# Optimization experiments

Hardware: AMD Instinct MI355X
Metric: run time of the kernel (lower is better)

The kernel has to match this reference:

```python
import jax, jax.numpy as jnp
import numpy as np

B, NA, NT, P, DA, DM, H = 1, 4096, 1024, 32768, 128, 512, 4
DH = DA // H
DF = 4 * DA
WINDOW = 16


def _layer_norm(x, g=None, b=None, eps=1e-5):
    m = jnp.mean(x, axis=-1, keepdims=True)
    v = jnp.var(x, axis=-1, keepdims=True)
    xn = (x - m) / jnp.sqrt(v + eps)
    if g is not None:
        xn = xn * g + b
    return xn


def setup_inputs() -> dict:
    key = jax.random.key(0)
    ks = jax.random.split(key, 32)
    r = lambda k, s: (jax.random.normal(k, s, dtype=jnp.float32) * 0.05)
    return {
        'q': r(ks[0], (B, NA, DA)),
        'c_atom': r(ks[1], (B, NA, DA)),
        'h_cond': r(ks[2], (B, NT, DM)),
        'p_lm': r(ks[3], (B, P, 16)),
        't_emb': r(ks[4], (B, DA)),
        'cond_proj_w': r(ks[5], (DM, DA)), 'cond_proj_b': r(ks[6], (DA,)),
        'adaln1_w': r(ks[7], (DA, 2 * DA)), 'adaln1_b': r(ks[8], (2 * DA,)),
        'adaln2_w': r(ks[9], (DA, 2 * DA)), 'adaln2_b': r(ks[10], (2 * DA,)),
        'ln_g': jnp.ones((DA,), jnp.float32), 'ln_b': jnp.zeros((DA,), jnp.float32),
        'wq': r(ks[11], (DA, DA)), 'wk': r(ks[12], (DA, DA)),
        'wv': r(ks[13], (DA, DA)), 'wg': r(ks[14], (DA, DA)),
        'wo': r(ks[15], (DA, DA)),
        'pair_w': r(ks[16], (16, H)), 'pair_b': r(ks[17], (H,)),
        'gate1_w': r(ks[18], (DA, DA)), 'gate1_b': r(ks[19], (DA,)),
        'gate2_w': r(ks[20], (DA, DA)), 'gate2_b': r(ks[21], (DA,)),
        'sw1': r(ks[22], (DA, DF)), 'sw3': r(ks[23], (DA, DF)),
        'sw2': r(ks[24], (DF, DA)),
        'p_lm_idx': jax.random.randint(ks[25], (B, P, 2), 0, NA, dtype=jnp.int32),
        'token_idx': jnp.sort(jax.random.randint(ks[26], (B, NA), 0, NT, dtype=jnp.int32), axis=-1),
    }


def _forward(q, c_atom, h_cond, p_lm, t_emb,
             cond_proj_w, cond_proj_b, adaln1_w, adaln1_b, adaln2_w, adaln2_b,
             ln_g, ln_b, wq, wk, wv, wg, wo, pair_w, pair_b,
             gate1_w, gate1_b, gate2_w, gate2_b, sw1, sw3, sw2,
             p_lm_idx, token_idx):
    Bq, N, D = q.shape
    # gather token conditioning to atoms: (B, NA, DM)
    h_atoms = jax.vmap(lambda h, t: h[t])(h_cond, token_idx)
    cond = t_emb[:, None, :] + h_atoms @ cond_proj_w + cond_proj_b  # (B, NA, DA)
    g1, b1 = jnp.split(cond @ adaln1_w + adaln1_b, 2, axis=-1)
    q_n = (1.0 + g1) * _layer_norm(q, ln_g, ln_b) + b1

    Q = (q_n @ wq).reshape(Bq, N, H, DH)
    K = (q_n @ wk).reshape(Bq, N, H, DH)
    V = (q_n @ wv).reshape(Bq, N, H, DH)
    G_flat = q_n @ wg  # (B, N, DA); permute/reshape in torch is identity on layout

    scores = jnp.einsum('bihd,bjhd->bhij', Q, K) / jnp.sqrt(jnp.float32(DH))

    # scattered pair bias: (B, P, H) -> dense (B, H, N, N)
    bias = p_lm @ pair_w + pair_b  # (B, P, H)

    def scat(idx, bb):
        return jnp.zeros((N, N, H), bb.dtype).at[idx[:, 0], idx[:, 1]].set(bb)

    pair_bias = jax.vmap(scat)(p_lm_idx, bias).transpose(0, 3, 1, 2)
    scores = scores + pair_bias

    pos = jnp.arange(N)
    window = jnp.abs(pos[:, None] - pos[None, :]) <= WINDOW  # (N, N)
    scores = jnp.where(window[None, None, :, :], scores, -jnp.inf)

    attn = jax.nn.softmax(scores, axis=-1)
    att_out = jnp.einsum('bhij,bjhd->bihd', attn, V).reshape(Bq, N, D)

    q1 = q + jax.nn.sigmoid(G_flat) * (att_out @ wo)
    q1 = q1 + jax.nn.sigmoid(c_atom @ gate1_w + gate1_b) * q1

    g2, b2 = jnp.split(cond @ adaln2_w + adaln2_b, 2, axis=-1)
    q_n2 = (1.0 + g2) * _layer_norm(q1) + b2
    swi = (jax.nn.silu(q_n2 @ sw1) * (q_n2 @ sw3)) @ sw2
    q2 = q1 + jax.nn.sigmoid(c_atom @ gate2_w + gate2_b) * swi
    return q2  # atom_pad_mask is all-ones -> final mask multiply is identity


def reference(q, c_atom, h_cond, p_lm, t_emb,
              cond_proj_w, cond_proj_b, adaln1_w, adaln1_b, adaln2_w, adaln2_b,
              ln_g, ln_b, wq, wk, wv, wg, wo, pair_w, pair_b,
              gate1_w, gate1_b, gate2_w, gate2_b, sw1, sw3, sw2,
              p_lm_idx, token_idx):
    return _forward(q, c_atom, h_cond, p_lm, t_emb,
                    cond_proj_w, cond_proj_b, adaln1_w, adaln1_b, adaln2_w, adaln2_b,
                    ln_g, ln_b, wq, wk, wv, wg, wo, pair_w, pair_b,
                    gate1_w, gate1_b, gate2_w, gate2_b, sw1, sw3, sw2,
                    p_lm_idx, token_idx)
```

## Files before the change

kernel.cpp:

```cpp
#include <hip/hip_runtime.h>
#include <math.h>

#define NA   4096
#define DA   128
#define DM   512
#define NT   1024
#define HH   4
#define DF   512
#define PP   32768
#define WIN  16
#define BAND 33
#define KSTR 132

typedef __attribute__((ext_vector_type(8))) short bf16x8;
typedef __attribute__((ext_vector_type(4))) float f32x4;

__device__ __forceinline__ float sigmoidf_(float x) { return 1.0f / (1.0f + __expf(-x)); }
__device__ __forceinline__ ushort f2bf(float f) {
    union { float f; unsigned int i; } x; x.f = f;
    unsigned int r = x.i + 0x7fffu + ((x.i >> 16) & 1u);
    return (ushort)(r >> 16);
}

__global__ __launch_bounds__(256) void k_prep(
    const float* __restrict__ hc, const float* __restrict__ ca,
    const float* __restrict__ cw, const float* __restrict__ a1, const float* __restrict__ a2,
    const float* __restrict__ wq, const float* __restrict__ wk, const float* __restrict__ wv,
    const float* __restrict__ wg, const float* __restrict__ wo,
    const float* __restrict__ g1, const float* __restrict__ g2,
    const float* __restrict__ s1, const float* __restrict__ s3, const float* __restrict__ s2,
    ushort* hcb, ushort* cab, ushort* cwT, ushort* a1T, ushort* a2T,
    ushort* wqT, ushort* wkT, ushort* wvT, ushort* wgT, ushort* woT,
    ushort* g1T, ushort* g2T, ushort* s1T, ushort* s3T, ushort* s2T,
    float* band)
{
    __shared__ float tile[32][33];
    const int y = blockIdx.y, bx = blockIdx.x, tid = threadIdx.x;
    if (y <= 1) {
        const float4* src = (const float4*)(y == 0 ? hc : ca);
        ushort* dst = y == 0 ? hcb : cab;
        for (int i = bx * 256 + tid; i < 131072; i += 16384) {
            float4 v = src[i];
            ushort4 st; st.x = f2bf(v.x); st.y = f2bf(v.y); st.z = f2bf(v.z); st.w = f2bf(v.w);
            *(ushort4*)&dst[(size_t)i * 4] = st;
        }
        return;
    }
    if (y == 15) {
        float4 z = {0.f, 0.f, 0.f, 0.f};
        float4* b4 = (float4*)band;
        for (int i = bx * 256 + tid; i < 135168; i += 16384) b4[i] = z;
        return;
    }
    const float* src; ushort* dst; int K, N;
    switch (y) {
        case 2:  src = cw; dst = cwT; K = 512; N = 128; break;
        case 3:  src = a1; dst = a1T; K = 128; N = 256; break;
        case 4:  src = a2; dst = a2T; K = 128; N = 256; break;
        case 5:  src = wq; dst = wqT; K = 128; N = 128; break;
        case 6:  src = wk; dst = wkT; K = 128; N = 128; break;
        case 7:  src = wv; dst = wvT; K = 128; N = 128; break;
        case 8:  src = wg; dst = wgT; K = 128; N = 128; break;
        case 9:  src = wo; dst = woT; K = 128; N = 128; break;
        case 10: src = g1; dst = g1T; K = 128; N = 128; break;
        case 11: src = g2; dst = g2T; K = 128; N = 128; break;
        case 12: src = s1; dst = s1T; K = 128; N = 512; break;
        case 13: src = s3; dst = s3T; K = 128; N = 512; break;
        default: src = s2; dst = s2T; K = 512; N = 128; break;
    }
    const int tn_cnt = N >> 5;
    if (bx >= (K >> 5) * tn_cnt) return;
    const int k0 = (bx / tn_cnt) << 5, n0 = (bx % tn_cnt) << 5;
    {
        int r = tid >> 3, c = (tid & 7) << 2;
        float4 v = *(const float4*)&src[(size_t)(k0 + r) * N + n0 + c];
        tile[r][c + 0] = v.x; tile[r][c + 1] = v.y;
        tile[r][c + 2] = v.z; tile[r][c + 3] = v.w;
    }
    __syncthreads();
    {
        int rn = tid >> 3, ck = (tid & 7) << 2;
        ushort4 st;
        st.x = f2bf(tile[ck + 0][rn]);
        st.y = f2bf(tile[ck + 1][rn]);
        st.z = f2bf(tile[ck + 2][rn]);
        st.w = f2bf(tile[ck + 3][rn]);
        *(ushort4*)&dst[(size_t)(n0 + rn) * K + k0 + ck] = st;
    }
}

__global__ __launch_bounds__(256) void k_condmod(
    const ushort* __restrict__ hcb, const int* __restrict__ tok,
    const ushort* __restrict__ cwT, const float* __restrict__ t_emb,
    const float* __restrict__ cond_b, const ushort* __restrict__ cab,
    const ushort* __restrict__ a1T, const ushort* __restrict__ a2T,
    const ushort* __restrict__ g1T, const ushort* __restrict__ g2T,
    const float* __restrict__ ad1b, const float* __restrict__ ad2b,
    const float* __restrict__ g1b, const float* __restrict__ g2b,
    const float* __restrict__ p_lm, const float* __restrict__ pair_w,
    const float* __restrict__ pair_b, const int* __restrict__ p_idx,
    float* __restrict__ band,
    float* __restrict__ gb1, float* __restrict__ gb2,
    float* __restrict__ gate1, float* __restrict__ gate2)
{
    const int tid = threadIdx.x, b = blockIdx.x;
    if (b >= 256) {
        int p = (b - 256) * 256 + tid;
        int i = p_idx[2 * p], j = p_idx[2 * p + 1];
        int d = j - i + WIN;
        if (d < 0 || d > 2 * WIN) return;
        float v0 = pair_b[0], v1 = pair_b[1], v2 = pair_b[2], v3 = pair_b[3];
        #pragma unroll
        for (int k = 0; k < 16; ++k) {
            float a = p_lm[p * 16 + k];
            v0 = fmaf(a, pair_w[k * 4 + 0], v0);
            v1 = fmaf(a, pair_w[k * 4 + 1], v1);
            v2 = fmaf(a, pair_w[k * 4 + 2], v2);
            v3 = fmaf(a, pair_w[k * 4 + 3], v3);
        }
        size_t base = ((size_t)i * HH) * BAND + d;
        band[base + 0 * BAND] = v0;
        band[base + 1 * BAND] = v1;
        band[base + 2 * BAND] = v2;
        band[base + 3 * BAND] = v3;
        return;
    }
    __shared__ ushort cond_s[16 * 128];
    const int l = tid & 63, wv = tid >> 6;
    const int cl = l & 15, kq = l >> 4, ko = kq * 8;
    const int r0 = b * 16;
    {
        const int n0 = wv * 32;
        const ushort* Arow = hcb + (size_t)tok[r0 + cl] * DM;
        const ushort* Wc = cwT + (size_t)(n0 + cl) * DM;
        f32x4 acc[2] = {};
        #pragma unroll
        for (int ks = 0; ks < 16; ++ks) {
            bf16x8 a = *(const bf16x8*)(Arow + ks * 32 + ko);
            #pragma unroll
            for (int nf = 0; nf < 2; ++nf) {
                bf16x8 bb = *(const bf16x8*)(Wc + (size_t)nf * 16 * DM + ks * 32 + ko);
                acc[nf] = __builtin_amdgcn_mfma_f32_16x16x32_bf16(a, bb, acc[nf], 0, 0, 0);
            }
        }
        #pragma unroll
        for (int nf = 0; nf < 2; ++nf) {
            int col = n0 + nf * 16 + cl;
            float add = t_emb[col] + cond_b[col];
            #pragma unroll
            for (int r = 0; r < 4; ++r) {
                int row = kq * 4 + r;
                int byte = row * 256 + col * 2;
                byte ^= (row & 7) << 4;
                *(ushort*)((char*)cond_s + byte) = f2bf(acc[nf][r] + add);
            }
        }
    }
    __syncthreads();
    {
        const int n0 = wv * 64;
        const ushort* W1c = a1T + (size_t)(n0 + cl) * DA;
        const ushort* W2c = a2T + (size_t)(n0 + cl) * DA;
        f32x4 acc1[4] = {}, acc2[4] = {};
        #pragma unroll
        for (int ks = 0; ks < 4; ++ks) {
            int byteA = cl * 256 + (ks * 32 + ko) * 2;
            byteA ^= (cl & 7) << 4;
            bf16x8 a = *(const bf16x8*)((char*)cond_s + byteA);
            #pragma unroll
            for (int nf = 0; nf < 4; ++nf) {
                bf16x8 b1 = *(const bf16x8*)(W1c + (size_t)nf * 16 * DA + ks * 32 + ko);
                acc1[nf] = __builtin_amdgcn_mfma_f32_16x16x32_bf16(a, b1, acc1[nf], 0, 0, 0);
                bf16x8 b2 = *(const bf16x8*)(W2c + (size_t)nf * 16 * DA + ks * 32 + ko);
                acc2[nf] = __builtin_amdgcn_mfma_f32_16x16x32_bf16(a, b2, acc2[nf], 0, 0, 0);
            }
        }
        #pragma unroll
        for (int nf = 0; nf < 4; ++nf) {
            int col = n0 + nf * 16 + cl;
            float b1v = ad1b[col], b2v = ad2b[col];
            #pragma unroll
            for (int r = 0; r < 4; ++r) {
                size_t rc = (size_t)(r0 + kq * 4 + r) * 256 + col;
                gb1[rc] = acc1[nf][r] + b1v;
                gb2[rc] = acc2[nf][r] + b2v;
            }
        }
    }
    {
        const int n0 = wv * 32;
        const ushort* Arow = cab + (size_t)(r0 + cl) * DA;
        const ushort* W1c = g1T + (size_t)(n0 + cl) * DA;
        const ushort* W2c = g2T + (size_t)(n0 + cl) * DA;
        f32x4 acc1[2] = {}, acc2[2] = {};
        #pragma unroll
        for (int ks = 0; ks < 4; ++ks) {
            bf16x8 a = *(const bf16x8*)(Arow + ks * 32 + ko);
            #pragma unroll
            for (int nf = 0; nf < 2; ++nf) {
                bf16x8 b1 = *(const bf16x8*)(W1c + (size_t)nf * 16 * DA + ks * 32 + ko);
                acc1[nf] = __builtin_amdgcn_mfma_f32_16x16x32_bf16(a, b1, acc1[nf], 0, 0, 0);
                bf16x8 b2 = *(const bf16x8*)(W2c + (size_t)nf * 16 * DA + ks * 32 + ko);
                acc2[nf] = __builtin_amdgcn_mfma_f32_16x16x32_bf16(a, b2, acc2[nf], 0, 0, 0);
            }
        }
        #pragma unroll
        for (int nf = 0; nf < 2; ++nf) {
            int col = n0 + nf * 16 + cl;
            float b1v = g1b[col], b2v = g2b[col];
            #pragma unroll
            for (int r = 0; r < 4; ++r) {
                size_t rc = (size_t)(r0 + kq * 4 + r) * DA + col;
                gate1[rc] = sigmoidf_(acc1[nf][r] + b1v);
                gate2[rc] = sigmoidf_(acc2[nf][r] + b2v);
            }
        }
    }
}

__global__ __launch_bounds__(512) void k_mega(
    const float* __restrict__ qg, const float* __restrict__ gb1,
    const float* __restrict__ gb2, const float* __restrict__ gate1,
    const float* __restrict__ gate2, const float* __restrict__ ln_g,
    const float* __restrict__ ln_b, const float* __restrict__ band,
    const ushort* __restrict__ wqT, const ushort* __restrict__ wkT,
    const ushort* __restrict__ wvT, const ushort* __restrict__ wgT,
    const ushort* __restrict__ woT, const ushort* __restrict__ s1T,
    const ushort* __restrict__ s3T, const ushort* __restrict__ s2T,
    float* __restrict__ out)
{
    __shared__ ushort qn_s[48 * 128];
    __shared__ float  K_s[48 * KSTR];
    __shared__ float  V_s[48 * KSTR];
    __shared__ float  Q_s[16 * KSTR];
    __shared__ float  sG_s[16 * KSTR];
    __shared__ float  q1_s[16 * KSTR];
    __shared__ ushort att_s[16 * 128];
    __shared__ ushort hb_s[16 * 512];

    const int tid = threadIdx.x;
    const int l = tid & 63, wv = tid >> 6;
    const int cl = l & 15, kq = l >> 4, ko = kq * 8;
    const int r0 = blockIdx.x * 16;
    const int hb0 = r0 - 16;

    #pragma unroll
    for (int rr = 0; rr < 6; ++rr) {
        int hr = wv * 6 + rr;
        int gr = hb0 + hr;
        ushort2 st = {0, 0};
        if ((unsigned)gr < NA) {
            float2 xv = *(const float2*)&qg[(size_t)gr * DA + 2 * l];
            float sum = xv.x + xv.y, sq = xv.x * xv.x + xv.y * xv.y;
            #pragma unroll
            for (int off = 1; off <= 32; off <<= 1) {
                sum += __shfl_xor(sum, off);
                sq  += __shfl_xor(sq,  off);
            }
            float m = sum * (1.0f / DA);
            float rs = rsqrtf(sq * (1.0f / DA) - m * m + 1e-5f);
            float2 g = *(const float2*)&gb1[(size_t)gr * 256 + 2 * l];
            float2 bb = *(const float2*)&gb1[(size_t)gr * 256 + 128 + 2 * l];
            float2 lg = *(const float2*)&ln_g[2 * l];
            float2 lb = *(const float2*)&ln_b[2 * l];
            float xn0 = (xv.x - m) * rs * lg.x + lb.x;
            float xn1 = (xv.y - m) * rs * lg.y + lb.y;
            st.x = f2bf((1.f + g.x) * xn0 + bb.x);
            st.y = f2bf((1.f + g.y) * xn1 + bb.y);
        }
        int byte = hr * 256 + 4 * l;
        byte ^= (hr & 7) << 4;
        *(ushort2*)((char*)qn_s + byte) = st;
    }
    __syncthreads();

    {
        int t, isV = 0;
        const ushort* WT;
        if (wv < 6) { t = wv >> 1; isV = wv & 1; WT = isV ? wvT : wkT; }
        else        { t = 1; WT = (wv == 6) ? wqT : wgT; }
        const ushort* Wc = WT + (size_t)cl * DA;
        f32x4 acc[8] = {};
        #pragma unroll
        for (int ks = 0; ks < 4; ++ks) {
            int byteA = (t * 16 + cl) * 256 + (ks * 32 + ko) * 2;
            byteA ^= (cl & 7) << 4;
            bf16x8 a = *(const bf16x8*)((char*)qn_s + byteA);
            #pragma unroll
            for (int nf = 0; nf < 8; ++nf) {
                bf16x8 b = *(const bf16x8*)(Wc + (size_t)nf * 16 * DA + ks * 32 + ko);
                acc[nf] = __builtin_amdgcn_mfma_f32_16x16x32_bf16(a, b, acc[nf], 0, 0, 0);
            }
        }
        if (wv < 6) {
            float* dst = isV ? V_s : K_s;
            #pragma unroll
            for (int nf = 0; nf < 8; ++nf)
                #pragma unroll
                for (int r = 0; r < 4; ++r)
                    dst[(t * 16 + kq * 4 + r) * KSTR + nf * 16 + cl] = acc[nf][r];
        } else if (wv == 6) {
            #pragma unroll
            for (int nf = 0; nf < 8; ++nf)
                #pragma unroll
                for (int r = 0; r < 4; ++r)
                    Q_s[(kq * 4 + r) * KSTR + nf * 16 + cl] = acc[nf][r];
        } else {
            #pragma unroll
            for (int nf = 0; nf < 8; ++nf)
                #pragma unroll
                for (int r = 0; r < 4; ++r)
                    sG_s[(kq * 4 + r) * KSTR + nf * 16 + cl] = sigmoidf_(acc[nf][r]);
        }
    }
    __syncthreads();

    {
        const int g = tid >> 3, l3 = tid & 7;
        const int rl = g >> 2, h = g & 3;
        const int gr = r0 + rl;
        const float scale = 0.17677669529663687f;
        float4 qr0 = *(const float4*)&Q_s[rl * KSTR + h * 32 + l3 * 4];
        const float* brow = band + ((size_t)gr * HH + h) * BAND;
        float s[BAND];
        float m = -1e30f;
        #pragma unroll
        for (int jo = 0; jo < BAND; ++jo) {
            int j = gr - WIN + jo;
            float sv = -1e30f;
            if ((unsigned)j < NA) {
                float4 kk = *(const float4*)&K_s[(rl + jo) * KSTR + h * 32 + l3 * 4];
                float d = 0.f;
                d = fmaf(qr0.x, kk.x, d); d = fmaf(qr0.y, kk.y, d);
                d = fmaf(qr0.z, kk.z, d); d = fmaf(qr0.w, kk.w, d);
                d += __shfl_xor(d, 1);
                d += __shfl_xor(d, 2);
                d += __shfl_xor(d, 4);
                sv = fmaf(d, scale, brow[jo]);
            }
            s[jo] = sv;
            m = fmaxf(m, sv);
        }
        float lsum = 0.f;
        #pragma unroll
        for (int jo = 0; jo < BAND; ++jo) {
            float p = __expf(s[jo] - m);
            s[jo] = p;
            lsum += p;
        }
        float inv = 1.0f / lsum;
        float4 o = {0.f, 0.f, 0.f, 0.f};
        #pragma unroll
        for (int jo = 0; jo < BAND; ++jo) {
            int j = gr - WIN + jo;
            if ((unsigned)j < NA) {
                float4 v = *(const float4*)&V_s[(rl + jo) * KSTR + h * 32 + l3 * 4];
                o.x = fmaf(s[jo], v.x, o.x);
                o.y = fmaf(s[jo], v.y, o.y);
                o.z = fmaf(s[jo], v.z, o.z);
                o.w = fmaf(s[jo], v.w, o.w);
            }
        }
        ushort4 st;
        st.x = f2bf(o.x * inv); st.y = f2bf(o.y * inv);
        st.z = f2bf(o.z * inv); st.w = f2bf(o.w * inv);
        int byte = rl * 256 + h * 64 + l3 * 8;
        byte ^= (rl & 7) << 4;
        *(ushort4*)((char*)att_s + byte) = st;
    }
    __syncthreads();

    {
        const int n0 = wv * 16;
        const ushort* Wc = woT + (size_t)(n0 + cl) * DA;
        f32x4 acc = {0.f, 0.f, 0.f, 0.f};
        #pragma unroll
        for (int ks = 0; ks < 4; ++ks) {
            int byteA = cl * 256 + (ks * 32 + ko) * 2;
            byteA ^= (cl & 7) << 4;
            bf16x8 a = *(const bf16x8*)((char*)att_s + byteA);
            bf16x8 b = *(const bf16x8*)(Wc + ks * 32 + ko);
            acc = __builtin_amdgcn_mfma_f32_16x16x32_bf16(a, b, acc, 0, 0, 0);
        }
        #pragma unroll
        for (int r = 0; r < 4; ++r) {
            int row = kq * 4 + r;
            int gr = r0 + row, col = n0 + cl;
            float qv = qg[(size_t)gr * DA + col];
            float sg = sG_s[row * KSTR + col];
            float g1v = gate1[(size_t)gr * DA + col];
            q1_s[row * KSTR + col] = (qv + sg * acc[r]) * (1.f + g1v);
        }
    }
    __syncthreads();

    bf16x8 afr[4];
    {
        const int row = cl, gr = r0 + cl;
        float qv2[4][8];
        float sum = 0.f, sq = 0.f;
        #pragma unroll
        for (int ks = 0; ks < 4; ++ks) {
            float4 v0 = *(const float4*)&q1_s[row * KSTR + ks * 32 + ko];
            float4 v1 = *(const float4*)&q1_s[row * KSTR + ks * 32 + ko + 4];
            qv2[ks][0] = v0.x; qv2[ks][1] = v0.y; qv2[ks][2] = v0.z; qv2[ks][3] = v0.w;
            qv2[ks][4] = v1.x; qv2[ks][5] = v1.y; qv2[ks][6] = v1.z; qv2[ks][7] = v1.w;
            sum += v0.x + v0.y + v0.z + v0.w + v1.x + v1.y + v1.z + v1.w;
            sq += v0.x * v0.x + v0.y * v0.y + v0.z * v0.z + v0.w * v0.w
                + v1.x * v1.x + v1.y * v1.y + v1.z * v1.z + v1.w * v1.w;
        }
        sum += __shfl_xor(sum, 16); sq += __shfl_xor(sq, 16);
        sum += __shfl_xor(sum, 32); sq += __shfl_xor(sq, 32);
        float mean = sum * (1.0f / DA);
        float rs = rsqrtf(sq * (1.0f / DA) - mean * mean + 1e-5f);
        #pragma unroll
        for (int ks = 0; ks < 4; ++ks) {
            int k = ks * 32 + ko;
            float4 g0 = *(const float4*)&gb2[(size_t)gr * 256 + k];
            float4 g1v = *(const float4*)&gb2[(size_t)gr * 256 + k + 4];
            float4 b0 = *(const float4*)&gb2[(size_t)gr * 256 + 128 + k];
            float4 b1v = *(const float4*)&gb2[(size_t)gr * 256 + 128 + k + 4];
            float gg[8] = {g0.x, g0.y, g0.z, g0.w, g1v.x, g1v.y, g1v.z, g1v.w};
            float bb[8] = {b0.x, b0.y, b0.z, b0.w, b1v.x, b1v.y, b1v.z, b1v.w};
            #pragma unroll
            for (int j = 0; j < 8; ++j) {
                float xn = (qv2[ks][j] - mean) * rs;
                afr[ks][j] = (short)f2bf((1.f + gg[j]) * xn + bb[j]);
            }
        }
    }

    {
        const int c0 = wv * 64;
        const ushort* W1 = s1T + (size_t)(c0 + cl) * DA;
        const ushort* W3 = s3T + (size_t)(c0 + cl) * DA;
        f32x4 acc1[4] = {}, acc3[4] = {};
        #pragma unroll
        for (int ks = 0; ks < 4; ++ks) {
            #pragma unroll
            for (int nf = 0; nf < 4; ++nf) {
                bf16x8 b1 = *(const bf16x8*)(W1 + (size_t)nf * 16 * DA + ks * 32 + ko);
                acc1[nf] = __builtin_amdgcn_mfma_f32_16x16x32_bf16(afr[ks], b1, acc1[nf], 0, 0, 0);
                bf16x8 b3 = *(const bf16x8*)(W3 + (size_t)nf * 16 * DA + ks * 32 + ko);
                acc3[nf] = __builtin_amdgcn_mfma_f32_16x16x32_bf16(afr[ks], b3, acc3[nf], 0, 0, 0);
            }
        }
        #pragma unroll
        for (int nf = 0; nf < 4; ++nf) {
            #pragma unroll
            for (int r = 0; r < 4; ++r) {
                float x1 = acc1[nf][r], x3 = acc3[nf][r];
                float h = x1 * sigmoidf_(x1) * x3;
                int rr = kq * 4 + r;
                int col = c0 + nf * 16 + cl;
                int byte = rr * 1024 + col * 2;
                byte ^= (rr & 7) << 4;
                *(ushort*)((char*)hb_s + byte) = f2bf(h);
            }
        }
    }
    __syncthreads();
    {
        const int n0 = wv * 16;
        const ushort* W2 = s2T + (size_t)(n0 + cl) * DF;
        f32x4 acc = {0.f, 0.f, 0.f, 0.f};
        #pragma unroll
        for (int ks = 0; ks < 16; ++ks) {
            int byteA = cl * 1024 + (ks * 32 + ko) * 2;
            byteA ^= (cl & 7) << 4;
            bf16x8 a = *(const bf16x8*)((char*)hb_s + byteA);
            bf16x8 b = *(const bf16x8*)(W2 + ks * 32 + ko);
            acc = __builtin_amdgcn_mfma_f32_16x16x32_bf16(a, b, acc, 0, 0, 0);
        }
        #pragma unroll
        for (int r = 0; r < 4; ++r) {
            int row = kq * 4 + r;
            int gr = r0 + row, col = n0 + cl;
            size_t rc = (size_t)gr * DA + col;
            out[rc] = q1_s[row * KSTR + col] + gate2[rc] * acc[r];
        }
    }
}

extern "C" void kernel_launch(void* const* d_in, const int* in_sizes, int n_in,
                              void* d_out, int out_size, void* d_ws, size_t ws_size,
                              hipStream_t stream)
{
    const float* q      = (const float*)d_in[0];
    const float* c_atom = (const float*)d_in[1];
    const float* h_cond = (const float*)d_in[2];
    const float* p_lm   = (const float*)d_in[3];
    const float* t_emb  = (const float*)d_in[4];
    const float* cond_w = (const float*)d_in[5];
    const float* cond_b = (const float*)d_in[6];
    const float* ad1w   = (const float*)d_in[7];
    const float* ad1b   = (const float*)d_in[8];
    const float* ad2w   = (const float*)d_in[9];
    const float* ad2b   = (const float*)d_in[10];
    const float* ln_g   = (const float*)d_in[11];
    const float* ln_b   = (const float*)d_in[12];
    const float* wq     = (const float*)d_in[13];
    const float* wk     = (const float*)d_in[14];
    const float* wv     = (const float*)d_in[15];
    const float* wg     = (const float*)d_in[16];
    const float* wo     = (const float*)d_in[17];
    const float* pair_w = (const float*)d_in[18];
    const float* pair_b = (const float*)d_in[19];
    const float* g1w    = (const float*)d_in[20];
    const float* g1b    = (const float*)d_in[21];
    const float* g2w    = (const float*)d_in[22];
    const float* g2b    = (const float*)d_in[23];
    const float* sw1    = (const float*)d_in[24];
    const float* sw3    = (const float*)d_in[25];
    const float* sw2    = (const float*)d_in[26];
    const int*   p_idx  = (const int*)d_in[27];
    const int*   tok    = (const int*)d_in[28];
    float* out = (float*)d_out;

    size_t off = 0;
    char* base = (char*)d_ws;
    auto alloc = [&](size_t bytes) -> void* {
        void* p = base + off;
        off += (bytes + 255) & ~(size_t)255;
        return p;
    };
    ushort* hcb     = (ushort*)alloc((size_t)NT * DM * 2);
    ushort* cab     = (ushort*)alloc((size_t)NA * DA * 2);
    ushort* cwT     = (ushort*)alloc((size_t)DM * DA * 2);
    ushort* a1T     = (ushort*)alloc((size_t)256 * 128 * 2);
    ushort* a2T     = (ushort*)alloc((size_t)256 * 128 * 2);
    ushort* wqT     = (ushort*)alloc((size_t)128 * 128 * 2);
    ushort* wkT     = (ushort*)alloc((size_t)128 * 128 * 2);
    ushort* wvT     = (ushort*)alloc((size_t)128 * 128 * 2);
    ushort* wgT     = (ushort*)alloc((size_t)128 * 128 * 2);
    ushort* woT     = (ushort*)alloc((size_t)128 * 128 * 2);
    ushort* g1T     = (ushort*)alloc((size_t)128 * 128 * 2);
    ushort* g2T     = (ushort*)alloc((size_t)128 * 128 * 2);
    ushort* s1T     = (ushort*)alloc((size_t)512 * 128 * 2);
    ushort* s3T     = (ushort*)alloc((size_t)512 * 128 * 2);
    ushort* s2T     = (ushort*)alloc((size_t)128 * 512 * 2);
    float*  gb1     = (float*)alloc((size_t)NA * 256 * 4);
    float*  gb2     = (float*)alloc((size_t)NA * 256 * 4);
    float*  gate1   = (float*)alloc((size_t)NA * DA * 4);
    float*  gate2   = (float*)alloc((size_t)NA * DA * 4);
    float*  band    = (float*)alloc((size_t)NA * HH * BAND * 4);

    k_prep<<<dim3(64, 16), 256, 0, stream>>>(
        h_cond, c_atom, cond_w, ad1w, ad2w, wq, wk, wv, wg, wo,
        g1w, g2w, sw1, sw3, sw2,
        hcb, cab, cwT, a1T, a2T, wqT, wkT, wvT, wgT, woT,
        g1T, g2T, s1T, s3T, s2T, band);
    k_condmod<<<384, 256, 0, stream>>>(
        hcb, tok, cwT, t_emb, cond_b, cab,
        a1T, a2T, g1T, g2T, ad1b, ad2b, g1b, g2b,
        p_lm, pair_w, pair_b, p_idx, band,
        gb1, gb2, gate1, gate2);
    k_mega<<<256, 512, 0, stream>>>(
        q, gb1, gb2, gate1, gate2, ln_g, ln_b, band,
        wqT, wkT, wvT, wgT, woT, s1T, s3T, s2T, out);
    (void)in_sizes; (void)n_in; (void)out_size; (void)ws_size;
}
```

Measured before the change: 168.5 us.

## Fuse input bf16 conversion into condmod, store adaLN in bf16, stage mega inputs in LDS

Drops the separate h_cond/c_atom bf16 conversion pass in k_prep and converts fp32 rows on the fly inside k_condmod. The adaLN gamma/beta intermediates are written as bf16 to halve their traffic. k_mega now bulk-loads q, gb1/gb2, gates and band rows into a large shared pool up front, stores K/V as bf16 in LDS, and splits LayerNorm into a stats pass plus a vectorized normalize pass. The ~160KB LDS pool limits occupancy to one block per CU and adds precision loss in the adaLN and K/V values.

```diff
diff --git a/kernel.cpp b/kernel.cpp
--- a/kernel.cpp
+++ b/kernel.cpp
@@ -10,7 +10,6 @@
 #define PP   32768
 #define WIN  16
 #define BAND 33
-#define KSTR 132
 
 typedef __attribute__((ext_vector_type(8))) short bf16x8;
 typedef __attribute__((ext_vector_type(4))) float f32x4;
@@ -21,32 +20,27 @@
     unsigned int r = x.i + 0x7fffu + ((x.i >> 16) & 1u);
     return (ushort)(r >> 16);
 }
+__device__ __forceinline__ float bf2f(ushort u) {
+    union { unsigned int i; float f; } x; x.i = ((unsigned int)u) << 16;
+    return x.f;
+}
+
+#define MFMA(a, b, c) __builtin_amdgcn_mfma_f32_16x16x32_bf16((a), (b), (c), 0, 0, 0)
 
 __global__ __launch_bounds__(256) void k_prep(
-    const float* __restrict__ hc, const float* __restrict__ ca,
     const float* __restrict__ cw, const float* __restrict__ a1, const float* __restrict__ a2,
     const float* __restrict__ wq, const float* __restrict__ wk, const float* __restrict__ wv,
     const float* __restrict__ wg, const float* __restrict__ wo,
     const float* __restrict__ g1, const float* __restrict__ g2,
     const float* __restrict__ s1, const float* __restrict__ s3, const float* __restrict__ s2,
-    ushort* hcb, ushort* cab, ushort* cwT, ushort* a1T, ushort* a2T,
+    ushort* cwT, ushort* a1T, ushort* a2T,
     ushort* wqT, ushort* wkT, ushort* wvT, ushort* wgT, ushort* woT,
     ushort* g1T, ushort* g2T, ushort* s1T, ushort* s3T, ushort* s2T,
     float* band)
 {
     __shared__ float tile[32][33];
     const int y = blockIdx.y, bx = blockIdx.x, tid = threadIdx.x;
-    if (y <= 1) {
-        const float4* src = (const float4*)(y == 0 ? hc : ca);
-        ushort* dst = y == 0 ? hcb : cab;
-        for (int i = bx * 256 + tid; i < 131072; i += 16384) {
-            float4 v = src[i];
-            ushort4 st; st.x = f2bf(v.x); st.y = f2bf(v.y); st.z = f2bf(v.z); st.w = f2bf(v.w);
-            *(ushort4*)&dst[(size_t)i * 4] = st;
-        }
-        return;
-    }
-    if (y == 15) {
+    if (y == 13) {
         float4 z = {0.f, 0.f, 0.f, 0.f};
         float4* b4 = (float4*)band;
         for (int i = bx * 256 + tid; i < 135168; i += 16384) b4[i] = z;
@@ -54,18 +48,18 @@
     }
     const float* src; ushort* dst; int K, N;
     switch (y) {
-        case 2:  src = cw; dst = cwT; K = 512; N = 128; break;
-        case 3:  src = a1; dst = a1T; K = 128; N = 256; break;
-        case 4:  src = a2; dst = a2T; K = 128; N = 256; break;
-        case 5:  src = wq; dst = wqT; K = 128; N = 128; break;
-        case 6:  src = wk; dst = wkT; K = 128; N = 128; break;
-        case 7:  src = wv; dst = wvT; K = 128; N = 128; break;
-        case 8:  src = wg; dst = wgT; K = 128; N = 128; break;
-        case 9:  src = wo; dst = woT; K = 128; N = 128; break;
-        case 10: src = g1; dst = g1T; K = 128; N = 128; break;
-        case 11: src = g2; dst = g2T; K = 128; N = 128; break;
-        case 12: src = s1; dst = s1T; K = 128; N = 512; break;
-        case 13: src = s3; dst = s3T; K = 128; N = 512; break;
+        case 0:  src = cw; dst = cwT; K = 512; N = 128; break;
+        case 1:  src = a1; dst = a1T; K = 128; N = 256; break;
+        case 2:  src = a2; dst = a2T; K = 128; N = 256; break;
+        case 3:  src = wq; dst = wqT; K = 128; N = 128; break;
+        case 4:  src = wk; dst = wkT; K = 128; N = 128; break;
+        case 5:  src = wv; dst = wvT; K = 128; N = 128; break;
+        case 6:  src = wg; dst = wgT; K = 128; N = 128; break;
+        case 7:  src = wo; dst = woT; K = 128; N = 128; break;
+        case 8:  src = g1; dst = g1T; K = 128; N = 128; break;
+        case 9:  src = g2; dst = g2T; K = 128; N = 128; break;
+        case 10: src = s1; dst = s1T; K = 128; N = 512; break;
+        case 11: src = s3; dst = s3T; K = 128; N = 512; break;
         default: src = s2; dst = s2T; K = 512; N = 128; break;
     }
     const int tn_cnt = N >> 5;
@@ -90,9 +84,9 @@
 }
 
 __global__ __launch_bounds__(256) void k_condmod(
-    const ushort* __restrict__ hcb, const int* __restrict__ tok,
+    const float* __restrict__ h_cond, const int* __restrict__ tok,
     const ushort* __restrict__ cwT, const float* __restrict__ t_emb,
-    const float* __restrict__ cond_b, const ushort* __restrict__ cab,
+    const float* __restrict__ cond_b, const float* __restrict__ c_atom,
     const ushort* __restrict__ a1T, const ushort* __restrict__ a2T,
     const ushort* __restrict__ g1T, const ushort* __restrict__ g2T,
     const float* __restrict__ ad1b, const float* __restrict__ ad2b,
@@ -100,7 +94,7 @@
     const float* __restrict__ p_lm, const float* __restrict__ pair_w,
     const float* __restrict__ pair_b, const int* __restrict__ p_idx,
     float* __restrict__ band,
-    float* __restrict__ gb1, float* __restrict__ gb2,
+    ushort* __restrict__ gb1, ushort* __restrict__ gb2,
     float* __restrict__ gate1, float* __restrict__ gate2)
 {
     const int tid = threadIdx.x, b = blockIdx.x;
@@ -130,17 +124,23 @@
     const int cl = l & 15, kq = l >> 4, ko = kq * 8;
     const int r0 = b * 16;
     {
+        const float* Arow = h_cond + (size_t)tok[r0 + cl] * DM;
         const int n0 = wv * 32;
-        const ushort* Arow = hcb + (size_t)tok[r0 + cl] * DM;
         const ushort* Wc = cwT + (size_t)(n0 + cl) * DM;
         f32x4 acc[2] = {};
         #pragma unroll
         for (int ks = 0; ks < 16; ++ks) {
-            bf16x8 a = *(const bf16x8*)(Arow + ks * 32 + ko);
+            float4 x0 = *(const float4*)(Arow + ks * 32 + ko);
+            float4 x1 = *(const float4*)(Arow + ks * 32 + ko + 4);
+            bf16x8 a;
+            a[0] = (short)f2bf(x0.x); a[1] = (short)f2bf(x0.y);
+            a[2] = (short)f2bf(x0.z); a[3] = (short)f2bf(x0.w);
+            a[4] = (short)f2bf(x1.x); a[5] = (short)f2bf(x1.y);
+            a[6] = (short)f2bf(x1.z); a[7] = (short)f2bf(x1.w);
             #pragma unroll
             for (int nf = 0; nf < 2; ++nf) {
                 bf16x8 bb = *(const bf16x8*)(Wc + (size_t)nf * 16 * DM + ks * 32 + ko);
-                acc[nf] = __builtin_amdgcn_mfma_f32_16x16x32_bf16(a, bb, acc[nf], 0, 0, 0);
+                acc[nf] = MFMA(a, bb, acc[nf]);
             }
         }
         #pragma unroll
@@ -170,9 +170,9 @@
             #pragma unroll
             for (int nf = 0; nf < 4; ++nf) {
                 bf16x8 b1 = *(const bf16x8*)(W1c + (size_t)nf * 16 * DA + ks * 32 + ko);
-                acc1[nf] = __builtin_amdgcn_mfma_f32_16x16x32_bf16(a, b1, acc1[nf], 0, 0, 0);
+                acc1[nf] = MFMA(a, b1, acc1[nf]);
                 bf16x8 b2 = *(const bf16x8*)(W2c + (size_t)nf * 16 * DA + ks * 32 + ko);
-                acc2[nf] = __builtin_amdgcn_mfma_f32_16x16x32_bf16(a, b2, acc2[nf], 0, 0, 0);
+                acc2[nf] = MFMA(a, b2, acc2[nf]);
             }
         }
         #pragma unroll
@@ -182,26 +182,32 @@
             #pragma unroll
             for (int r = 0; r < 4; ++r) {
                 size_t rc = (size_t)(r0 + kq * 4 + r) * 256 + col;
-                gb1[rc] = acc1[nf][r] + b1v;
-                gb2[rc] = acc2[nf][r] + b2v;
-            }
-        }
-    }
-    {
+                gb1[rc] = f2bf(acc1[nf][r] + b1v);
+                gb2[rc] = f2bf(acc2[nf][r] + b2v);
+            }
+        }
+    }
+    {
+        const float* Arow = c_atom + (size_t)(r0 + cl) * DA;
         const int n0 = wv * 32;
-        const ushort* Arow = cab + (size_t)(r0 + cl) * DA;
         const ushort* W1c = g1T + (size_t)(n0 + cl) * DA;
         const ushort* W2c = g2T + (size_t)(n0 + cl) * DA;
         f32x4 acc1[2] = {}, acc2[2] = {};
         #pragma unroll
         for (int ks = 0; ks < 4; ++ks) {
-            bf16x8 a = *(const bf16x8*)(Arow + ks * 32 + ko);
+            float4 x0 = *(const float4*)(Arow + ks * 32 + ko);
+            float4 x1 = *(const float4*)(Arow + ks * 32 + ko + 4);
+            bf16x8 a;
+            a[0] = (short)f2bf(x0.x); a[1] = (short)f2bf(x0.y);
+            a[2] = (short)f2bf(x0.z); a[3] = (short)f2bf(x0.w);
+            a[4] = (short)f2bf(x1.x); a[5] = (short)f2bf(x1.y);
+            a[6] = (short)f2bf(x1.z); a[7] = (short)f2bf(x1.w);
             #pragma unroll
             for (int nf = 0; nf < 2; ++nf) {
                 bf16x8 b1 = *(const bf16x8*)(W1c + (size_t)nf * 16 * DA + ks * 32 + ko);
-                acc1[nf] = __builtin_amdgcn_mfma_f32_16x16x32_bf16(a, b1, acc1[nf], 0, 0, 0);
+                acc1[nf] = MFMA(a, b1, acc1[nf]);
                 bf16x8 b2 = *(const bf16x8*)(W2c + (size_t)nf * 16 * DA + ks * 32 + ko);
-                acc2[nf] = __builtin_amdgcn_mfma_f32_16x16x32_bf16(a, b2, acc2[nf], 0, 0, 0);
+                acc2[nf] = MFMA(a, b2, acc2[nf]);
             }
         }
         #pragma unroll
@@ -219,24 +225,33 @@
 }
 
 __global__ __launch_bounds__(512) void k_mega(
-    const float* __restrict__ qg, const float* __restrict__ gb1,
-    const float* __restrict__ gb2, const float* __restrict__ gate1,
-    const float* __restrict__ gate2, const float* __restrict__ ln_g,
-    const float* __restrict__ ln_b, const float* __restrict__ band,
+    const float* __restrict__ qg, const ushort* __restrict__ gb1g,
+    const ushort* __restrict__ gb2g, const float* __restrict__ gate1g,
+    const float* __restrict__ gate2g, const float* __restrict__ ln_g,
+    const float* __restrict__ ln_b, const float* __restrict__ bandg,
     const ushort* __restrict__ wqT, const ushort* __restrict__ wkT,
     const ushort* __restrict__ wvT, const ushort* __restrict__ wgT,
     const ushort* __restrict__ woT, const ushort* __restrict__ s1T,
     const ushort* __restrict__ s3T, const ushort* __restrict__ s2T,
     float* __restrict__ out)
 {
-    __shared__ ushort qn_s[48 * 128];
-    __shared__ float  K_s[48 * KSTR];
-    __shared__ float  V_s[48 * KSTR];
-    __shared__ float  Q_s[16 * KSTR];
-    __shared__ float  sG_s[16 * KSTR];
-    __shared__ float  q1_s[16 * KSTR];
-    __shared__ ushort att_s[16 * 128];
-    __shared__ ushort hb_s[16 * 512];
+    __shared__ __align__(16) char pool[162944];
+    float*  q_s     = (float*)(pool + 0);
+    ushort* gb1_s   = (ushort*)(pool + 25344);
+    ushort* gb2_s   = (ushort*)(pool + 50304);
+    float*  gate1_s = (float*)(pool + 58624);
+    float*  gate2_s = (float*)(pool + 67072);
+    float*  band_s  = (float*)(pool + 75520);
+    float*  mu_s    = (float*)(pool + 83968);
+    float*  rs_s    = (float*)(pool + 84160);
+    char*   qn_c    = pool + 84352;
+    char*   K_c     = pool + 96640;
+    char*   V_c     = pool + 108928;
+    float*  Q_s     = (float*)(pool + 121216);
+    float*  sG_s    = (float*)(pool + 129664);
+    float*  q1_s    = (float*)(pool + 138112);
+    char*   att_c   = pool + 146560;
+    char*   hb_c    = pool + 146560;
 
     const int tid = threadIdx.x;
     const int l = tid & 63, wv = tid >> 6;
@@ -244,33 +259,74 @@
     const int r0 = blockIdx.x * 16;
     const int hb0 = r0 - 16;
 
+    for (int i = tid; i < 48 * 32; i += 512) {
+        int r = i >> 5, c = (i & 31) << 2;
+        int gr = hb0 + r; int grc = gr < 0 ? 0 : (gr >= NA ? NA - 1 : gr);
+        *(float4*)&q_s[r * 132 + c] = *(const float4*)&qg[(size_t)grc * DA + c];
+    }
+    for (int i = tid; i < 48 * 64; i += 512) {
+        int r = i >> 6, c = (i & 63) << 2;
+        int gr = hb0 + r; int grc = gr < 0 ? 0 : (gr >= NA ? NA - 1 : gr);
+        *(ushort4*)&gb1_s[r * 260 + c] = *(const ushort4*)&gb1g[(size_t)grc * 256 + c];
+    }
+    for (int i = tid; i < 16 * 64; i += 512) {
+        int r = i >> 6, c = (i & 63) << 2;
+        *(ushort4*)&gb2_s[r * 260 + c] = *(const ushort4*)&gb2g[(size_t)(r0 + r) * 256 + c];
+    }
+    for (int i = tid; i < 16 * 32; i += 512) {
+        int r = i >> 5, c = (i & 31) << 2;
+        *(float4*)&gate1_s[r * 132 + c] = *(const float4*)&gate1g[(size_t)(r0 + r) * DA + c];
+        *(float4*)&gate2_s[r * 132 + c] = *(const float4*)&gate2g[(size_t)(r0 + r) * DA + c];
+    }
+    for (int i = tid; i < 16 * 33; i += 512) {
+        int r = i >> 5, c = (i & 31) << 2;
+        if ((i & 31) < 32) {
+            *(float4*)&band_s[r * 132 + c] = *(const float4*)&bandg[(size_t)(r0 + r) * 132 + c];
+        }
+    }
+    if (tid < 16) {
+        *(float4*)&band_s[tid * 132 + 128] = *(const float4*)&bandg[(size_t)(r0 + tid) * 132 + 128];
+    }
+    __syncthreads();
+
     #pragma unroll
     for (int rr = 0; rr < 6; ++rr) {
         int hr = wv * 6 + rr;
-        int gr = hb0 + hr;
-        ushort2 st = {0, 0};
-        if ((unsigned)gr < NA) {
-            float2 xv = *(const float2*)&qg[(size_t)gr * DA + 2 * l];
-            float sum = xv.x + xv.y, sq = xv.x * xv.x + xv.y * xv.y;
-            #pragma unroll
-            for (int off = 1; off <= 32; off <<= 1) {
-                sum += __shfl_xor(sum, off);
-                sq  += __shfl_xor(sq,  off);
-            }
+        float2 xv = *(const float2*)&q_s[hr * 132 + 2 * l];
+        float sum = xv.x + xv.y, sq = xv.x * xv.x + xv.y * xv.y;
+        #pragma unroll
+        for (int off = 1; off <= 32; off <<= 1) {
+            sum += __shfl_xor(sum, off);
+            sq  += __shfl_xor(sq,  off);
+        }
+        if (l == 0) {
             float m = sum * (1.0f / DA);
-            float rs = rsqrtf(sq * (1.0f / DA) - m * m + 1e-5f);
-            float2 g = *(const float2*)&gb1[(size_t)gr * 256 + 2 * l];
-            float2 bb = *(const float2*)&gb1[(size_t)gr * 256 + 128 + 2 * l];
-            float2 lg = *(const float2*)&ln_g[2 * l];
-            float2 lb = *(const float2*)&ln_b[2 * l];
-            float xn0 = (xv.x - m) * rs * lg.x + lb.x;
-            float xn1 = (xv.y - m) * rs * lg.y + lb.y;
-            st.x = f2bf((1.f + g.x) * xn0 + bb.x);
-            st.y = f2bf((1.f + g.y) * xn1 + bb.y);
-        }
-        int byte = hr * 256 + 4 * l;
-        byte ^= (hr & 7) << 4;
-        *(ushort2*)((char*)qn_s + byte) = st;
+            mu_s[hr] = m;
+            rs_s[hr] = rsqrtf(sq * (1.0f / DA) - m * m + 1e-5f);
+        }
+    }
+    __syncthreads();
+
+    for (int i = tid; i < 48 * 16; i += 512) {
+        int r = i >> 4, cg = (i & 15) * 8;
+        float mu = mu_s[r], rs = rs_s[r];
+        ushort4 o0, o1;
+        #pragma unroll
+        for (int j = 0; j < 8; ++j) {
+            float qv = q_s[r * 132 + cg + j];
+            float g = bf2f(gb1_s[r * 260 + cg + j]);
+            float bb = bf2f(gb1_s[r * 260 + 128 + cg + j]);
+            float xn = (qv - mu) * rs * ln_g[cg + j] + ln_b[cg + j];
+            ushort v = f2bf((1.f + g) * xn + bb);
+            if (j == 0) o0.x = v; else if (j == 1) o0.y = v;
+            else if (j == 2) o0.z = v; else if (j == 3) o0.w = v;
+            else if (j == 4) o1.x = v; else if (j == 5) o1.y = v;
+            else if (j == 6) o1.z = v; else o1.w = v;
+        }
+        int byte = r * 256 + cg * 2;
+        byte ^= (r & 7) << 4;
+        *(ushort4*)(qn_c + byte) = o0;
+        *(ushort4*)(qn_c + byte + 8) = o1;
     }
     __syncthreads();
 
@@ -285,32 +341,36 @@
         for (int ks = 0; ks < 4; ++ks) {
             int byteA = (t * 16 + cl) * 256 + (ks * 32 + ko) * 2;
             byteA ^= (cl & 7) << 4;
-            bf16x8 a = *(const bf16x8*)((char*)qn_s + byteA);
+            bf16x8 a = *(const bf16x8*)(qn_c + byteA);
             #pragma unroll
             for (int nf = 0; nf < 8; ++nf) {
                 bf16x8 b = *(const bf16x8*)(Wc + (size_t)nf * 16 * DA + ks * 32 + ko);
-                acc[nf] = __builtin_amdgcn_mfma_f32_16x16x32_bf16(a, b, acc[nf], 0, 0, 0);
+                acc[nf] = MFMA(a, b, acc[nf]);
             }
         }
         if (wv < 6) {
-            float* dst = isV ? V_s : K_s;
+            char* dst = isV ? V_c : K_c;
+            #pragma unroll
+            for (int nf = 0; nf < 8; ++nf)
+                #pragma unroll
+                for (int r = 0; r < 4; ++r) {
+                    int row = t * 16 + kq * 4 + r;
+                    int byte = row * 256 + (nf * 16 + cl) * 2;
+                    byte ^= (row & 7) << 4;
+                    *(ushort*)(dst + byte) = f2bf(acc[nf][r]);
+                }
+        } else if (wv == 6) {
             #pragma unroll
             for (int nf = 0; nf < 8; ++nf)
                 #pragma unroll
                 for (int r = 0; r < 4; ++r)
-                    dst[(t * 16 + kq * 4 + r) * KSTR + nf * 16 + cl] = acc[nf][r];
-        } else if (wv == 6) {
+                    Q_s[(kq * 4 + r) * 132 + nf * 16 + cl] = acc[nf][r];
+        } else {
             #pragma unroll
             for (int nf = 0; nf < 8; ++nf)
                 #pragma unroll
                 for (int r = 0; r < 4; ++r)
-                    Q_s[(kq * 4 + r) * KSTR + nf * 16 + cl] = acc[nf][r];
-        } else {
-            #pragma unroll
-            for (int nf = 0; nf < 8; ++nf)
-                #pragma unroll
-                for (int r = 0; r < 4; ++r)
-                    sG_s[(kq * 4 + r) * KSTR + nf * 16 + cl] = sigmoidf_(acc[nf][r]);
+                    sG_s[(kq * 4 + r) * 132 + nf * 16 + cl] = sigmoidf_(acc[nf][r]);
         }
     }
     __syncthreads();
@@ -320,8 +380,8 @@
         const int rl = g >> 2, h = g & 3;
         const int gr = r0 + rl;
         const float scale = 0.17677669529663687f;
-        float4 qr0 = *(const float4*)&Q_s[rl * KSTR + h * 32 + l3 * 4];
-        const float* brow = band + ((size_t)gr * HH + h) * BAND;
+        float4 qr0 = *(const float4*)&Q_s[rl * 132 + h * 32 + l3 * 4];
+        const float* brow = band_s + rl * 132 + h * BAND;
         float s[BAND];
         float m = -1e30f;
         #pragma unroll
@@ -329,10 +389,15 @@
             int j = gr - WIN + jo;
             float sv = -1e30f;
             if ((unsigned)j < NA) {
-                float4 kk = *(const float4*)&K_s[(rl + jo) * KSTR + h * 32 + l3 * 4];
+                int krow = rl + jo;
+                int byte = krow * 256 + (h * 32 + l3 * 4) * 2;
+                byte ^= (krow & 7) << 4;
+                ushort4 ku = *(const ushort4*)(K_c + byte);
                 float d = 0.f;
-                d = fmaf(qr0.x, kk.x, d); d = fmaf(qr0.y, kk.y, d);
-                d = fmaf(qr0.z, kk.z, d); d = fmaf(qr0.w, kk.w, d);
+                d = fmaf(qr0.x, bf2f(ku.x), d);
+                d = fmaf(qr0.y, bf2f(ku.y), d);
+                d = fmaf(qr0.z, bf2f(ku.z), d);
+                d = fmaf(qr0.w, bf2f(ku.w), d);
                 d += __shfl_xor(d, 1);
                 d += __shfl_xor(d, 2);
                 d += __shfl_xor(d, 4);
@@ -354,11 +419,14 @@
         for (int jo = 0; jo < BAND; ++jo) {
             int j = gr - WIN + jo;
             if ((unsigned)j < NA) {
-                float4 v = *(const float4*)&V_s[(rl + jo) * KSTR + h * 32 + l3 * 4];
-                o.x = fmaf(s[jo], v.x, o.x);
-                o.y = fmaf(s[jo], v.y, o.y);
-                o.z = fmaf(s[jo], v.z, o.z);
-                o.w = fmaf(s[jo], v.w, o.w);
+                int krow = rl + jo;
+                int byte = krow * 256 + (h * 32 + l3 * 4) * 2;
+                byte ^= (krow & 7) << 4;
+                ushort4 vu = *(const ushort4*)(V_c + byte);
+                o.x = fmaf(s[jo], bf2f(vu.x), o.x);
+                o.y = fmaf(s[jo], bf2f(vu.y), o.y);
+                o.z = fmaf(s[jo], bf2f(vu.z), o.z);
+                o.w = fmaf(s[jo], bf2f(vu.w), o.w);
             }
         }
         ushort4 st;
@@ -366,7 +434,7 @@
         st.z = f2bf(o.z * inv); st.w = f2bf(o.w * inv);
         int byte = rl * 256 + h * 64 + l3 * 8;
         byte ^= (rl & 7) << 4;
-        *(ushort4*)((char*)att_s + byte) = st;
+        *(ushort4*)(att_c + byte) = st;
     }
     __syncthreads();
 
@@ -378,31 +446,30 @@
         for (int ks = 0; ks < 4; ++ks) {
             int byteA = cl * 256 + (ks * 32 + ko) * 2;
             byteA ^= (cl & 7) << 4;
-            bf16x8 a = *(const bf16x8*)((char*)att_s + byteA);
+            bf16x8 a = *(const bf16x8*)(att_c + byteA);
             bf16x8 b = *(const bf16x8*)(Wc + ks * 32 + ko);
-            acc = __builtin_amdgcn_mfma_f32_16x16x32_bf16(a, b, acc, 0, 0, 0);
+            acc = MFMA(a, b, acc);
         }
         #pragma unroll
         for (int r = 0; r < 4; ++r) {
-            int row = kq * 4 + r;
-            int gr = r0 + row, col = n0 + cl;
-            float qv = qg[(size_t)gr * DA + col];
-            float sg = sG_s[row * KSTR + col];
-            float g1v = gate1[(size_t)gr * DA + col];
-            q1_s[row * KSTR + col] = (qv + sg * acc[r]) * (1.f + g1v);
+            int row = kq * 4 + r, col = n0 + cl;
+            float qv = q_s[(16 + row) * 132 + col];
+            float sg = sG_s[row * 132 + col];
+            float g1v = gate1_s[row * 132 + col];
+            q1_s[row * 132 + col] = (qv + sg * acc[r]) * (1.f + g1v);
         }
     }
     __syncthreads();
 
     bf16x8 afr[4];
     {
-        const int row = cl, gr = r0 + cl;
+        const int row = cl;
         float qv2[4][8];
         float sum = 0.f, sq = 0.f;
         #pragma unroll
         for (int ks = 0; ks < 4; ++ks) {
-            float4 v0 = *(const float4*)&q1_s[row * KSTR + ks * 32 + ko];
-            float4 v1 = *(const float4*)&q1_s[row * KSTR + ks * 32 + ko + 4];
+            float4 v0 = *(const float4*)&q1_s[row * 132 + ks * 32 + ko];
+            float4 v1 = *(const float4*)&q1_s[row * 132 + ks * 32 + ko + 4];
             qv2[ks][0] = v0.x; qv2[ks][1] = v0.y; qv2[ks][2] = v0.z; qv2[ks][3] = v0.w;
             qv2[ks][4] = v1.x; qv2[ks][5] = v1.y; qv2[ks][6] = v1.z; qv2[ks][7] = v1.w;
             sum += v0.x + v0.y + v0.z + v0.w + v1.x + v1.y + v1.z + v1.w;
@@ -416,12 +483,14 @@
         #pragma unroll
         for (int ks = 0; ks < 4; ++ks) {
             int k = ks * 32 + ko;
-            float4 g0 = *(const float4*)&gb2[(size_t)gr * 256 + k];
-            float4 g1v = *(const float4*)&gb2[(size_t)gr * 256 + k + 4];
-            float4 b0 = *(const float4*)&gb2[(size_t)gr * 256 + 128 + k];
-            float4 b1v = *(const float4*)&gb2[(size_t)gr * 256 + 128 + k + 4];
-            float gg[8] = {g0.x, g0.y, g0.z, g0.w, g1v.x, g1v.y, g1v.z, g1v.w};
-            float bb[8] = {b0.x, b0.y, b0.z, b0.w, b1v.x, b1v.y, b1v.z, b1v.w};
+            ushort4 g0 = *(const ushort4*)&gb2_s[row * 260 + k];
+            ushort4 g1u = *(const ushort4*)&gb2_s[row * 260 + k + 4];
+            ushort4 b0 = *(const ushort4*)&gb2_s[row * 260 + 128 + k];
+            ushort4 b1u = *(const ushort4*)&gb2_s[row * 260 + 128 + k + 4];
+            float gg[8] = {bf2f(g0.x), bf2f(g0.y), bf2f(g0.z), bf2f(g0.w),
+                           bf2f(g1u.x), bf2f(g1u.y), bf2f(g1u.z), bf2f(g1u.w)};
+            float bb[8] = {bf2f(b0.x), bf2f(b0.y), bf2f(b0.z), bf2f(b0.w),
+                           bf2f(b1u.x), bf2f(b1u.y), bf2f(b1u.z), bf2f(b1u.w)};
             #pragma unroll
             for (int j = 0; j < 8; ++j) {
                 float xn = (qv2[ks][j] - mean) * rs;
@@ -440,9 +509,9 @@
             #pragma unroll
             for (int nf = 0; nf < 4; ++nf) {
                 bf16x8 b1 = *(const bf16x8*)(W1 + (size_t)nf * 16 * DA + ks * 32 + ko);
-                acc1[nf] = __builtin_amdgcn_mfma_f32_16x16x32_bf16(afr[ks], b1, acc1[nf], 0, 0, 0);
+                acc1[nf] = MFMA(afr[ks], b1, acc1[nf]);
                 bf16x8 b3 = *(const bf16x8*)(W3 + (size_t)nf * 16 * DA + ks * 32 + ko);
-                acc3[nf] = __builtin_amdgcn_mfma_f32_16x16x32_bf16(afr[ks], b3, acc3[nf], 0, 0, 0);
+                acc3[nf] = MFMA(afr[ks], b3, acc3[nf]);
             }
         }
         #pragma unroll
@@ -455,7 +524,7 @@
                 int col = c0 + nf * 16 + cl;
                 int byte = rr * 1024 + col * 2;
                 byte ^= (rr & 7) << 4;
-                *(ushort*)((char*)hb_s + byte) = f2bf(h);
+                *(ushort*)(hb_c + byte) = f2bf(h);
             }
         }
     }
@@ -468,16 +537,15 @@
         for (int ks = 0; ks < 16; ++ks) {
             int byteA = cl * 1024 + (ks * 32 + ko) * 2;
             byteA ^= (cl & 7) << 4;
-            bf16x8 a = *(const bf16x8*)((char*)hb_s + byteA);
+            bf16x8 a = *(const bf16x8*)(hb_c + byteA);
             bf16x8 b = *(const bf16x8*)(W2 + ks * 32 + ko);
-            acc = __builtin_amdgcn_mfma_f32_16x16x32_bf16(a, b, acc, 0, 0, 0);
+            acc = MFMA(a, b, acc);
         }
         #pragma unroll
         for (int r = 0; r < 4; ++r) {
-            int row = kq * 4 + r;
-            int gr = r0 + row, col = n0 + cl;
-            size_t rc = (size_t)gr * DA + col;
-            out[rc] = q1_s[row * KSTR + col] + gate2[rc] * acc[r];
+            int row = kq * 4 + r, col = n0 + cl;
+            size_t rc = (size_t)(r0 + row) * DA + col;
+            out[rc] = q1_s[row * 132 + col] + gate2_s[row * 132 + col] * acc[r];
         }
     }
 }
@@ -524,34 +592,30 @@
         off += (bytes + 255) & ~(size_t)255;
         return p;
     };
-    ushort* hcb     = (ushort*)alloc((size_t)NT * DM * 2);
-    ushort* cab     = (ushort*)alloc((size_t)NA * DA * 2);
-    ushort* cwT     = (ushort*)alloc((size_t)DM * DA * 2);
-    ushort* a1T     = (ushort*)alloc((size_t)256 * 128 * 2);
-    ushort* a2T     = (ushort*)alloc((size_t)256 * 128 * 2);
-    ushort* wqT     = (ushort*)alloc((size_t)128 * 128 * 2);
-    ushort* wkT     = (ushort*)alloc((size_t)128 * 128 * 2);
-    ushort* wvT     = (ushort*)alloc((size_t)128 * 128 * 2);
-    ushort* wgT     = (ushort*)alloc((size_t)128 * 128 * 2);
-    ushort* woT     = (ushort*)alloc((size_t)128 * 128 * 2);
-    ushort* g1T     = (ushort*)alloc((size_t)128 * 128 * 2);
-    ushort* g2T     = (ushort*)alloc((size_t)128 * 128 * 2);
-    ushort* s1T     = (ushort*)alloc((size_t)512 * 128 * 2);
-    ushort* s3T     = (ushort*)alloc((size_t)512 * 128 * 2);
-    ushort* s2T     = (ushort*)alloc((size_t)128 * 512 * 2);
-    float*  gb1     = (float*)alloc((size_t)NA * 256 * 4);
-    float*  gb2     = (float*)alloc((size_t)NA * 256 * 4);
-    float*  gate1   = (float*)alloc((size_t)NA * DA * 4);
-    float*  gate2   = (float*)alloc((size_t)NA * DA * 4);
-    float*  band    = (float*)alloc((size_t)NA * HH * BAND * 4);
-
-    k_prep<<<dim3(64, 16), 256, 0, stream>>>(
-        h_cond, c_atom, cond_w, ad1w, ad2w, wq, wk, wv, wg, wo,
-        g1w, g2w, sw1, sw3, sw2,
-        hcb, cab, cwT, a1T, a2T, wqT, wkT, wvT, wgT, woT,
-        g1T, g2T, s1T, s3T, s2T, band);
+    ushort* cwT   = (ushort*)alloc((size_t)DM * DA * 2);
+    ushort* a1T   = (ushort*)alloc((size_t)256 * 128 * 2);
+    ushort* a2T   = (ushort*)alloc((size_t)256 * 128 * 2);
+    ushort* wqT   = (ushort*)alloc((size_t)128 * 128 * 2);
+    ushort* wkT   = (ushort*)alloc((size_t)128 * 128 * 2);
+    ushort* wvT   = (ushort*)alloc((size_t)128 * 128 * 2);
+    ushort* wgT   = (ushort*)alloc((size_t)128 * 128 * 2);
+    ushort* woT   = (ushort*)alloc((size_t)128 * 128 * 2);
+    ushort* g1T   = (ushort*)alloc((size_t)128 * 128 * 2);
+    ushort* g2T   = (ushort*)alloc((size_t)128 * 128 * 2);
+    ushort* s1T   = (ushort*)alloc((size_t)512 * 128 * 2);
+    ushort* s3T   = (ushort*)alloc((size_t)512 * 128 * 2);
+    ushort* s2T   = (ushort*)alloc((size_t)128 * 512 * 2);
+    ushort* gb1   = (ushort*)alloc((size_t)NA * 256 * 2);
+    ushort* gb2   = (ushort*)alloc((size_t)NA * 256 * 2);
+    float*  gate1 = (float*)alloc((size_t)NA * DA * 4);
+    float*  gate2 = (float*)alloc((size_t)NA * DA * 4);
+    float*  band  = (float*)alloc((size_t)NA * HH * BAND * 4);
+
+    k_prep<<<dim3(64, 14), 256, 0, stream>>>(
+        cond_w, ad1w, ad2w, wq, wk, wv, wg, wo, g1w, g2w, sw1, sw3, sw2,
+        cwT, a1T, a2T, wqT, wkT, wvT, wgT, woT, g1T, g2T, s1T, s3T, s2T, band);
     k_condmod<<<384, 256, 0, stream>>>(
-        hcb, tok, cwT, t_emb, cond_b, cab,
+        h_cond, tok, cwT, t_emb, cond_b, c_atom,
         a1T, a2T, g1T, g2T, ad1b, ad2b, g1b, g2b,
         p_lm, pair_w, pair_b, p_idx, band,
         gb1, gb2, gate1, gate2);
```

Measured after the change: 168.1 us. Within noise of the previous version (-0.2%).
